# Kernel optimization log

Measured on AMD Instinct MI355X. Metric: run time of the kernel, lower is better.

Reference implementation:

```python
import jax, jax.numpy as jnp
import numpy as np

N, IN_DIM, OUT_DIM, H, EDGE_DIM, E = 4096, 256, 256, 4, 64, 131072
HEAD_DIM = OUT_DIM // H
LN_EPS = 1e-5


def setup_inputs() -> dict:
    key = jax.random.key(0)
    ks = jax.random.split(key, 12)
    s_in = 1.0 / np.sqrt(IN_DIM)
    s_e = 1.0 / np.sqrt(EDGE_DIM)
    s_o = 1.0 / np.sqrt(OUT_DIM)
    return {
        "node_features": jax.random.normal(ks[0], (N, IN_DIM), jnp.float32),
        "adj_matrix": jax.random.uniform(ks[1], (N, N), jnp.float32),
        "edge_features": jax.random.normal(ks[2], (E, EDGE_DIM), jnp.float32),
        "edge_indices": jax.random.randint(ks[3], (E, 2), 0, N, dtype=jnp.int32),
        "Wq": jax.random.normal(ks[4], (IN_DIM, OUT_DIM), jnp.float32) * s_in,
        "bq": jnp.zeros((OUT_DIM,), jnp.float32),
        "Wk": jax.random.normal(ks[5], (IN_DIM, OUT_DIM), jnp.float32) * s_in,
        "bk": jnp.zeros((OUT_DIM,), jnp.float32),
        "Wv": jax.random.normal(ks[6], (IN_DIM, OUT_DIM), jnp.float32) * s_in,
        "bv": jnp.zeros((OUT_DIM,), jnp.float32),
        "We": jax.random.normal(ks[7], (EDGE_DIM, H), jnp.float32) * s_e,
        "be": jnp.zeros((H,), jnp.float32),
        "Wo": jax.random.normal(ks[8], (OUT_DIM, OUT_DIM), jnp.float32) * s_o,
        "bo": jnp.zeros((OUT_DIM,), jnp.float32),
        "ln_gamma": jnp.ones((OUT_DIM,), jnp.float32),
        "ln_beta": jnp.zeros((OUT_DIM,), jnp.float32),
    }


def reference(node_features, adj_matrix, edge_features, edge_indices,
              Wq, bq, Wk, bk, Wv, bv, We, be, Wo, bo, ln_gamma, ln_beta):
    n = node_features.shape[0]
    scale = np.float32(1.0 / np.sqrt(HEAD_DIM))
    Q = (node_features @ Wq + bq).reshape(n, H, HEAD_DIM)
    K = (node_features @ Wk + bk).reshape(n, H, HEAD_DIM)
    V = (node_features @ Wv + bv).reshape(n, H, HEAD_DIM)
    # scores[n, m, h] = <Q[n,h], K[m,h]> / sqrt(d)
    scores = jnp.einsum('nhd,mhd->nmh', Q, K) * scale
    scores = scores + adj_matrix[:, :, None] * 10.0
    # per-edge additive attention bias, scatter-added into (src, tgt) slots
    edge_attn = edge_features[:, :EDGE_DIM] @ We + be  # [E, H]
    scores = scores.at[edge_indices[:, 0], edge_indices[:, 1]].add(edge_attn)
    attn = jax.nn.softmax(scores, axis=1)  # over key nodes m
    out = jnp.einsum('nmh,mhd->nhd', attn, V).reshape(n, OUT_DIM)
    out = out @ Wo + bo
    x = out + node_features  # residual
    mu = jnp.mean(x, axis=-1, keepdims=True)
    var = jnp.mean((x - mu) ** 2, axis=-1, keepdims=True)
    return ln_gamma * (x - mu) * jax.lax.rsqrt(var + LN_EPS) + ln_beta
```

## Files before the change

kernel.cpp:

```cpp
#include <hip/hip_runtime.h>
#include <hip/hip_bf16.h>

typedef unsigned short u16;
typedef unsigned int u32;
typedef __attribute__((ext_vector_type(8))) short bf8;
typedef __attribute__((ext_vector_type(4))) float f4;

#define SCALE 0.125f
#define LN_EPS 1e-5f
#define WS_NEED 18485504UL

__device__ __forceinline__ float bf2f(u16 u) {
    union { u32 i; float f; } x; x.i = ((u32)u) << 16; return x.f;
}
__device__ __forceinline__ u16 f2bf(float f) {
    union { u32 i; float f; } x; x.f = f;
    u32 i = x.i;
    return (u16)((i + 0x7FFFu + ((i >> 16) & 1u)) >> 16);
}
__device__ __forceinline__ float ldf(const void* p, long i, int isf) {
    return isf ? ((const float*)p)[i] : bf2f(((const u16*)p)[i]);
}

__global__ void k_zero(int* p, int n) {
    int i = blockIdx.x * 256 + threadIdx.x;
    if (i < n) p[i] = 0;
}

__global__ void k_detect(const u32* __restrict__ w, int nwords, int* flag) {
    int hits = 0;
    for (int i = blockIdx.x * 256 + threadIdx.x; i < nwords; i += 64 * 256) {
        u32 v = w[i];
        if (((v >> 7) & 0xFFu) == 0xFFu) hits++;
        if (((v >> 23) & 0xFFu) == 0xFFu) hits++;
    }
    if (hits) atomicOr(flag, 1);
}

__global__ __launch_bounds__(256) void k_cvt_small(
    const void* bq, const void* bk, const void* bv, const void* bo,
    const void* g, const void* bt, const void* We, const void* be,
    u16* __restrict__ SB, const int* __restrict__ flag)
{
    int isf = flag[0];
    int t = threadIdx.x;
    SB[0 * 256 + t] = isf ? f2bf(((const float*)bq)[t]) : ((const u16*)bq)[t];
    SB[1 * 256 + t] = isf ? f2bf(((const float*)bk)[t]) : ((const u16*)bk)[t];
    SB[2 * 256 + t] = isf ? f2bf(((const float*)bv)[t]) : ((const u16*)bv)[t];
    SB[3 * 256 + t] = isf ? f2bf(((const float*)bo)[t]) : ((const u16*)bo)[t];
    SB[4 * 256 + t] = isf ? f2bf(((const float*)g)[t])  : ((const u16*)g)[t];
    SB[5 * 256 + t] = isf ? f2bf(((const float*)bt)[t]) : ((const u16*)bt)[t];
    SB[6 * 256 + t] = isf ? f2bf(((const float*)We)[t]) : ((const u16*)We)[t];
    if (t < 4)
        SB[7 * 256 + t] = isf ? f2bf(((const float*)be)[t]) : ((const u16*)be)[t];
}

__global__ __launch_bounds__(256) void k_transpose(const void* __restrict__ Wq,
    const void* __restrict__ Wk, const void* __restrict__ Wv, const void* __restrict__ Wo,
    u16* __restrict__ out, const int* __restrict__ flag)
{
    __shared__ u16 tile[32][33];
    int isf = flag[0];
    const void* src = blockIdx.z == 0 ? Wq : blockIdx.z == 1 ? Wk : blockIdx.z == 2 ? Wv : Wo;
    u16* dst = out + blockIdx.z * 65536;
    int r0 = blockIdx.x * 32, c0 = blockIdx.y * 32;
    int lr = threadIdx.x >> 5, lc = threadIdx.x & 31;
    #pragma unroll
    for (int rr = 0; rr < 4; rr++) {
        int r = rr * 8 + lr;
        long idx = (long)(r0 + r) * 256 + c0 + lc;
        tile[r][lc] = isf ? f2bf(((const float*)src)[idx]) : ((const u16*)src)[idx];
    }
    __syncthreads();
    #pragma unroll
    for (int rr = 0; rr < 4; rr++) {
        int r = rr * 8 + lr;
        dst[(c0 + r) * 256 + r0 + lc] = tile[lc][r];
    }
}

__global__ __launch_bounds__(256) void k_qkv(const void* __restrict__ X,
    const u16* __restrict__ WT, const u16* __restrict__ SB,
    u16* __restrict__ Qo, u16* __restrict__ Kp, u16* __restrict__ Vp,
    const int* __restrict__ flag)
{
    int tid = threadIdx.x, wave = tid >> 6, lane = tid & 63, quad = lane >> 4, c = lane & 15;
    int m0 = blockIdx.x * 16;
    int isf = flag[0];

    bf8 af[8];
    if (isf) {
        const float* Xf = (const float*)X;
        #pragma unroll
        for (int ks = 0; ks < 8; ks++) {
            const float* p = Xf + (long)(m0 + c) * 256 + ks * 32 + quad * 8;
            f4 a = *(const f4*)p, b = *(const f4*)(p + 4);
            bf8 t;
            #pragma unroll
            for (int j = 0; j < 4; j++) { t[j] = (short)f2bf(a[j]); t[j + 4] = (short)f2bf(b[j]); }
            af[ks] = t;
        }
    } else {
        #pragma unroll
        for (int ks = 0; ks < 8; ks++)
            af[ks] = *(const bf8*)((const u16*)X + (long)(m0 + c) * 256 + ks * 32 + quad * 8);
    }

    for (int which = 0; which < 3; which++) {
        const u16* Wp = WT + which * 65536;
        const u16* bias = SB + which * 256;

        f4 acc[4];
        #pragma unroll
        for (int t = 0; t < 4; t++) acc[t] = (f4){0.f, 0.f, 0.f, 0.f};

        #pragma unroll
        for (int ks = 0; ks < 8; ks++) {
            #pragma unroll
            for (int t = 0; t < 4; t++) {
                bf8 bfr = *(const bf8*)(Wp + (wave * 64 + t * 16 + c) * 256 + ks * 32 + quad * 8);
                acc[t] = __builtin_amdgcn_mfma_f32_16x16x32_bf16(af[ks], bfr, acc[t], 0, 0, 0);
            }
        }
        #pragma unroll
        for (int t = 0; t < 4; t++) {
            int n = wave * 64 + t * 16 + c;
            float bb = bf2f(bias[n]);
            #pragma unroll
            for (int r = 0; r < 4; r++) {
                int row = m0 + quad * 4 + r;
                float v = acc[t][r] + bb;
                u16 bv16 = f2bf(v);
                if (which == 0) {
                    Qo[(long)row * 256 + n] = bv16;
                } else if (which == 1) {
                    int mt = row >> 6, tk = (row >> 4) & 3, ck = row & 15;
                    int hh = n >> 6, kw = (n >> 5) & 1, q = (n >> 3) & 3, j = n & 7;
                    long idx = ((long)(((mt * 4 + hh) * 4 + tk) * 2 + kw) * 64 + q * 16 + ck) * 8 + j;
                    Kp[idx] = bv16;
                } else {
                    int hh = n >> 6, t2 = (n >> 4) & 3, c2 = n & 15;
                    int mt = row >> 6, mo = row & 63, hf = mo >> 5, q = (mo >> 3) & 3, j = mo & 7;
                    long idx = ((long)(((mt * 4 + hh) * 4 + t2) * 2 + hf) * 64 + q * 16 + c2) * 8 + j;
                    Vp[idx] = bv16;
                }
            }
        }
    }
}

__global__ void k_count(const int* __restrict__ EI, int* bcnt) {
    int e = blockIdx.x * 256 + threadIdx.x;
    int src = EI[2 * e], tgt = EI[2 * e + 1];
    atomicAdd(&bcnt[(src >> 4) * 64 + (tgt >> 6)], 1);
}

__global__ __launch_bounds__(256) void k_scan(const int* __restrict__ cntin,
                                              int* __restrict__ bptr, int* __restrict__ nextc)
{
    __shared__ int tot[256], base_l[256];
    int tid = threadIdx.x;
    int s = 0;
    int loc[64];
    #pragma unroll
    for (int j = 0; j < 64; j++) { loc[j] = cntin[tid * 64 + j]; s += loc[j]; }
    tot[tid] = s;
    __syncthreads();
    if (tid == 0) {
        int run = 0;
        for (int i = 0; i < 256; i++) { int t = tot[i]; base_l[i] = run; run += t; }
        bptr[16384] = run;
    }
    __syncthreads();
    int b = base_l[tid];
    #pragma unroll
    for (int j = 0; j < 64; j++) { bptr[tid * 64 + j] = b; nextc[tid * 64 + j] = b; b += loc[j]; }
}

__global__ __launch_bounds__(256) void k_fill(const void* __restrict__ EF,
    const int* __restrict__ EI, const u16* __restrict__ SB,
    int* __restrict__ nextc, int* __restrict__ csr_tq, float* __restrict__ csr_b,
    const int* __restrict__ flag)
{
    __shared__ float Wl[64][4];
    __shared__ float bel[4];
    int tid = threadIdx.x;
    int isf = flag[0];
    Wl[tid >> 2][tid & 3] = bf2f(SB[6 * 256 + tid]);
    if (tid < 4) bel[tid] = bf2f(SB[7 * 256 + tid]);
    __syncthreads();
    int e = blockIdx.x * 256 + tid;
    int src = EI[2 * e], tgt = EI[2 * e + 1];
    float ea0 = bel[0], ea1 = bel[1], ea2 = bel[2], ea3 = bel[3];
    if (isf) {
        const float* Ff = (const float*)EF + (long)e * 64;
        for (int d0 = 0; d0 < 64; d0 += 4) {
            f4 v = *(const f4*)(Ff + d0);
            #pragma unroll
            for (int j = 0; j < 4; j++) {
                float f = v[j];
                ea0 += f * Wl[d0 + j][0];
                ea1 += f * Wl[d0 + j][1];
                ea2 += f * Wl[d0 + j][2];
                ea3 += f * Wl[d0 + j][3];
            }
        }
    } else {
        const u16* Fb = (const u16*)EF + (long)e * 64;
        for (int d0 = 0; d0 < 64; d0 += 8) {
            bf8 v8 = *(const bf8*)(Fb + d0);
            #pragma unroll
            for (int j = 0; j < 8; j++) {
                float f = bf2f((u16)v8[j]);
                ea0 += f * Wl[d0 + j][0];
                ea1 += f * Wl[d0 + j][1];
                ea2 += f * Wl[d0 + j][2];
                ea3 += f * Wl[d0 + j][3];
            }
        }
    }
    int bucket = (src >> 4) * 64 + (tgt >> 6);
    int pos = atomicAdd(&nextc[bucket], 1);
    csr_tq[pos] = ((src & 15) << 16) | tgt;
    f4 bb = {ea0, ea1, ea2, ea3};
    *(f4*)(csr_b + (long)pos * 4) = bb;
}

__global__ __launch_bounds__(64, 4) void k_flash(
    const u16* __restrict__ Qb, const u16* __restrict__ Kp, const u16* __restrict__ Vp,
    const void* __restrict__ adj, const int* __restrict__ bptr,
    const int* __restrict__ csr_tq, const float* __restrict__ csr_b,
    float* __restrict__ AOacc, float* __restrict__ Lacc, const int* __restrict__ flag)
{
    __shared__ alignas(16) float EBs[16][68];

    int lane = threadIdx.x, quad = lane >> 4, c = lane & 15;
    int qt = blockIdx.x, h = blockIdx.y, ks = blockIdx.z;
    int n0 = qt * 16;
    int isf = flag[0];

    bf8 qf[2];
    #pragma unroll
    for (int kw = 0; kw < 2; kw++)
        qf[kw] = *(const bf8*)(Qb + (long)(n0 + c) * 256 + h * 64 + kw * 32 + quad * 8);

    float l_run = 0.f;
    f4 Oacc[4];
    #pragma unroll
    for (int t = 0; t < 4; t++) Oacc[t] = (f4){0.f, 0.f, 0.f, 0.f};

    int zr = lane >> 2, zc0 = (lane & 3) * 16;
    int addrA = ((2 * (quad & 1)) * 16 + c) * 4;
    int addrB = addrA + 64;
    int selLo = quad < 2;

    int mt0 = ks * 16;

    f4 z = (f4){0.f, 0.f, 0.f, 0.f};
    #pragma unroll
    for (int k = 0; k < 4; k++) *(f4*)(&EBs[zr][zc0 + k * 4]) = z;

    f4 adjc[4];
    #pragma unroll
    for (int t = 0; t < 4; t++) {
        int col = mt0 * 64 + t * 16 + quad * 4;
        if (isf) {
            adjc[t] = *(const f4*)((const float*)adj + (long)(n0 + c) * 4096 + col);
        } else {
            ushort4 u = *(const ushort4*)((const u16*)adj + (long)(n0 + c) * 4096 + col);
            adjc[t] = (f4){bf2f(u.x), bf2f(u.y), bf2f(u.z), bf2f(u.w)};
        }
    }

    int bi0 = 0, bi1 = 0, tq = 0, has = 0;
    float ebv = 0.f;

    for (int rel = 0; rel < 16; rel++) {
        int mt = mt0 + rel;

        if ((rel & 3) == 0) {
            int b = qt * 64 + mt;
            bi0 = bptr[b]; bi1 = bptr[b + 4];
            int ie = bi0 + lane;
            has = ie < bi1;
            tq = 0; ebv = 0.f;
            if (has) { tq = csr_tq[ie]; ebv = csr_b[(long)ie * 4 + h]; }
        }

        if (has && (((tq & 0xFFFF) >> 6) == mt))
            atomicAdd(&EBs[tq >> 16][tq & 63], ebv);
        if (bi1 > bi0 + 64) {
            for (int i = bi0 + 64 + lane; i < bi1; i += 64) {
                int tq2 = csr_tq[i];
                if (((tq2 & 0xFFFF) >> 6) == mt)
                    atomicAdd(&EBs[tq2 >> 16][tq2 & 63], csr_b[(long)i * 4 + h]);
            }
        }

        float sv[4][4];
        #pragma unroll
        for (int t = 0; t < 4; t++) {
            f4 acc = (f4){0.f, 0.f, 0.f, 0.f};
            #pragma unroll
            for (int kw = 0; kw < 2; kw++) {
                bf8 kfr = *(const bf8*)(Kp + ((long)(((mt * 4 + h) * 4 + t) * 2 + kw) * 64 + lane) * 8);
                acc = __builtin_amdgcn_mfma_f32_16x16x32_bf16(kfr, qf[kw], acc, 0, 0, 0);
            }
            #pragma unroll
            for (int r = 0; r < 4; r++)
                sv[t][r] = acc[r] * SCALE + adjc[t][r] * 10.f;
        }

        if (rel < 15) {
            int m0n = (mt + 1) * 64;
            #pragma unroll
            for (int t = 0; t < 4; t++) {
                int col = m0n + t * 16 + quad * 4;
                if (isf) {
                    adjc[t] = *(const f4*)((const float*)adj + (long)(n0 + c) * 4096 + col);
                } else {
                    ushort4 u = *(const ushort4*)((const u16*)adj + (long)(n0 + c) * 4096 + col);
                    adjc[t] = (f4){bf2f(u.x), bf2f(u.y), bf2f(u.z), bf2f(u.w)};
                }
            }
        }

        #pragma unroll
        for (int t = 0; t < 4; t++) {
            f4 e = *(const f4*)(&EBs[c][t * 16 + quad * 4]);
            #pragma unroll
            for (int r = 0; r < 4; r++) sv[t][r] += e[r];
        }
        #pragma unroll
        for (int k = 0; k < 4; k++) *(f4*)(&EBs[zr][zc0 + k * 4]) = z;

        u32 pw[8];
        float s = 0.f;
        #pragma unroll
        for (int t = 0; t < 4; t++) {
            float p0 = __expf(sv[t][0]);
            float p1 = __expf(sv[t][1]);
            float p2 = __expf(sv[t][2]);
            float p3 = __expf(sv[t][3]);
            s += (p0 + p1) + (p2 + p3);
            pw[2 * t]     = (u32)f2bf(p0) | ((u32)f2bf(p1) << 16);
            pw[2 * t + 1] = (u32)f2bf(p2) | ((u32)f2bf(p3) << 16);
        }
        l_run += s;

        union PF { u32 w[4]; bf8 v; } pf0, pf1;
        {
            u32 a00 = (u32)__builtin_amdgcn_ds_bpermute(addrA, (int)pw[0]);
            u32 a10 = (u32)__builtin_amdgcn_ds_bpermute(addrA, (int)pw[2]);
            u32 a01 = (u32)__builtin_amdgcn_ds_bpermute(addrA, (int)pw[1]);
            u32 a11 = (u32)__builtin_amdgcn_ds_bpermute(addrA, (int)pw[3]);
            u32 b00 = (u32)__builtin_amdgcn_ds_bpermute(addrB, (int)pw[0]);
            u32 b10 = (u32)__builtin_amdgcn_ds_bpermute(addrB, (int)pw[2]);
            u32 b01 = (u32)__builtin_amdgcn_ds_bpermute(addrB, (int)pw[1]);
            u32 b11 = (u32)__builtin_amdgcn_ds_bpermute(addrB, (int)pw[3]);
            pf0.w[0] = selLo ? a00 : a10;
            pf0.w[1] = selLo ? a01 : a11;
            pf0.w[2] = selLo ? b00 : b10;
            pf0.w[3] = selLo ? b01 : b11;
            u32 c00 = (u32)__builtin_amdgcn_ds_bpermute(addrA, (int)pw[4]);
            u32 c10 = (u32)__builtin_amdgcn_ds_bpermute(addrA, (int)pw[6]);
            u32 c01 = (u32)__builtin_amdgcn_ds_bpermute(addrA, (int)pw[5]);
            u32 c11 = (u32)__builtin_amdgcn_ds_bpermute(addrA, (int)pw[7]);
            u32 d00 = (u32)__builtin_amdgcn_ds_bpermute(addrB, (int)pw[4]);
            u32 d10 = (u32)__builtin_amdgcn_ds_bpermute(addrB, (int)pw[6]);
            u32 d01 = (u32)__builtin_amdgcn_ds_bpermute(addrB, (int)pw[5]);
            u32 d11 = (u32)__builtin_amdgcn_ds_bpermute(addrB, (int)pw[7]);
            pf1.w[0] = selLo ? c00 : c10;
            pf1.w[1] = selLo ? c01 : c11;
            pf1.w[2] = selLo ? d00 : d10;
            pf1.w[3] = selLo ? d01 : d11;
        }

        #pragma unroll
        for (int t = 0; t < 4; t++) {
            f4 o = Oacc[t];
            bf8 v0 = *(const bf8*)(Vp + ((long)(((mt * 4 + h) * 4 + t) * 2 + 0) * 64 + lane) * 8);
            o = __builtin_amdgcn_mfma_f32_16x16x32_bf16(pf0.v, v0, o, 0, 0, 0);
            bf8 v1 = *(const bf8*)(Vp + ((long)(((mt * 4 + h) * 4 + t) * 2 + 1) * 64 + lane) * 8);
            o = __builtin_amdgcn_mfma_f32_16x16x32_bf16(pf1.v, v1, o, 0, 0, 0);
            Oacc[t] = o;
        }
    }

    l_run += __shfl_xor(l_run, 16);
    l_run += __shfl_xor(l_run, 32);

    #pragma unroll
    for (int t = 0; t < 4; t++) {
        #pragma unroll
        for (int r = 0; r < 4; r++) {
            int q = quad * 4 + r;
            atomicAdd(&AOacc[(long)(n0 + q) * 256 + h * 64 + t * 16 + c], Oacc[t][r]);
        }
    }
    if (quad == 0)
        atomicAdd(&Lacc[(n0 + c) * 4 + h], l_run);
}

__global__ __launch_bounds__(256) void k_reduce(const float* __restrict__ AOacc,
    const float* __restrict__ Lacc, u16* __restrict__ AOb)
{
    int n = blockIdx.x, hd = threadIdx.x;
    float L = Lacc[n * 4 + (hd >> 6)];
    AOb[(long)n * 256 + hd] = f2bf(AOacc[(long)n * 256 + hd] / L);
}

__global__ __launch_bounds__(256) void k_outln(
    const u16* __restrict__ AOb, const u16* __restrict__ WoT, const u16* __restrict__ SB,
    const void* __restrict__ Xin, const void* __restrict__ gv, const void* __restrict__ bv,
    void* __restrict__ out, const int* __restrict__ flag)
{
    __shared__ float Xl[16][257];
    __shared__ float ps[16][17], pss[16][17];
    __shared__ float mu_l[16], ri_l[16];
    int tid = threadIdx.x, wave = tid >> 6, lane = tid & 63, quad = lane >> 4, c = lane & 15;
    int m0 = blockIdx.x * 16;
    int isf = flag[0];

    bf8 af[8];
    #pragma unroll
    for (int ks = 0; ks < 8; ks++)
        af[ks] = *(const bf8*)(AOb + (long)(m0 + c) * 256 + ks * 32 + quad * 8);

    f4 acc[4];
    #pragma unroll
    for (int t = 0; t < 4; t++) acc[t] = (f4){0.f, 0.f, 0.f, 0.f};

    #pragma unroll
    for (int ks = 0; ks < 8; ks++) {
        #pragma unroll
        for (int t = 0; t < 4; t++) {
            bf8 bfr = *(const bf8*)(WoT + (wave * 64 + t * 16 + c) * 256 + ks * 32 + quad * 8);
            acc[t] = __builtin_amdgcn_mfma_f32_16x16x32_bf16(af[ks], bfr, acc[t], 0, 0, 0);
        }
    }
    #pragma unroll
    for (int t = 0; t < 4; t++) {
        int n = wave * 64 + t * 16 + c;
        float bb = bf2f(SB[3 * 256 + n]);
        #pragma unroll
        for (int r = 0; r < 4; r++) {
            int q = quad * 4 + r;
            float res = ldf(Xin, (long)(m0 + q) * 256 + n, isf);
            Xl[q][n] = acc[t][r] + bb + res;
        }
    }
    __syncthreads();
    int q = tid >> 4, i = tid & 15;
    float s = 0.f, ss = 0.f;
    #pragma unroll
    for (int j = 0; j < 16; j++) { float v = Xl[q][i * 16 + j]; s += v; ss += v * v; }
    ps[q][i] = s; pss[q][i] = ss;
    __syncthreads();
    if (tid < 16) {
        float s2 = 0.f, ss2 = 0.f;
        #pragma unroll
        for (int i2 = 0; i2 < 16; i2++) { s2 += ps[tid][i2]; ss2 += pss[tid][i2]; }
        float mu = s2 * (1.f / 256.f);
        float var = ss2 * (1.f / 256.f) - mu * mu;
        mu_l[tid] = mu;
        ri_l[tid] = rsqrtf(var + LN_EPS);
    }
    __syncthreads();
    float mu = mu_l[q], ri = ri_l[q];
    #pragma unroll
    for (int j = 0; j < 16; j++) {
        int n2 = i * 16 + j;
        float v = (Xl[q][n2] - mu) * ri;
        float g = ldf(gv, n2, isf), bt = ldf(bv, n2, isf);
        float y = g * v + bt;
        long oidx = (long)(m0 + q) * 256 + n2;
        if (isf) ((float*)out)[oidx] = y;
        else     ((u16*)out)[oidx] = f2bf(y);
    }
}

extern "C" void kernel_launch(void* const* d_in, const int* in_sizes, int n_in,
                              void* d_out, int out_size, void* d_ws, size_t ws_size,
                              hipStream_t stream)
{
    const void* node = d_in[0];
    const void* adj  = d_in[1];
    const void* ef   = d_in[2];
    const int*  ei   = (const int*)d_in[3];
    const void* Wq = d_in[4];  const void* bq = d_in[5];
    const void* Wk = d_in[6];  const void* bk = d_in[7];
    const void* Wv = d_in[8];  const void* bv = d_in[9];
    const void* We = d_in[10]; const void* be = d_in[11];
    const void* Wo = d_in[12]; const void* bo = d_in[13];
    const void* gamma = d_in[14];
    const void* beta  = d_in[15];

    if (ws_size < WS_NEED) return;

    char* ws = (char*)d_ws;
    u16*   WT     = (u16*)(ws + 0);
    u16*   Qb     = (u16*)(ws + 524288);
    u16*   AOb    = (u16*)(ws + 524288);
    u16*   Kp     = (u16*)(ws + 2621440);
    u16*   Vp     = (u16*)(ws + 4718592);
    float* AOacc  = (float*)(ws + 6815744);
    float* Lacc   = (float*)(ws + 11010048);
    u16*   SB     = (u16*)(ws + 15728640);
    int*   bcnt   = (int*)(ws + 15732736);
    int*   flag   = bcnt + 16384;
    int*   bptr   = (int*)(ws + 15798400);
    int*   csr_tq = (int*)(ws + 15864064);
    float* csr_b  = (float*)(ws + 16388352);

    k_zero<<<65, 256, 0, stream>>>(bcnt, 16416);
    k_zero<<<4160, 256, 0, stream>>>((int*)AOacc, 1064960);
    k_detect<<<64, 256, 0, stream>>>((const u32*)node, 524288, flag);
    k_cvt_small<<<1, 256, 0, stream>>>(bq, bk, bv, bo, gamma, beta, We, be, SB, flag);
    k_transpose<<<dim3(8, 8, 4), 256, 0, stream>>>(Wq, Wk, Wv, Wo, WT, flag);
    k_qkv<<<256, 256, 0, stream>>>(node, WT, SB, Qb, Kp, Vp, flag);
    k_count<<<512, 256, 0, stream>>>(ei, bcnt);
    k_scan<<<1, 256, 0, stream>>>(bcnt, bptr, bcnt);
    k_fill<<<512, 256, 0, stream>>>(ef, ei, SB, bcnt, csr_tq, csr_b, flag);
    k_flash<<<dim3(256, 4, 4), 64, 0, stream>>>(Qb, Kp, Vp, adj, bptr, csr_tq, csr_b,
                                                AOacc, Lacc, flag);
    k_reduce<<<4096, 256, 0, stream>>>(AOacc, Lacc, AOb);
    k_outln<<<256, 256, 0, stream>>>(AOb, WT + 3 * 65536, SB, node, gamma, beta, d_out, flag);
}
```

Baseline: 293.7 us.

## Fuse setup kernels, merge QKV with edge fill, prefetch K tiles in flash

Merges several small launches: the two zeroing kernels, format detection with edge counting, bias conversion into the transpose, and the QKV projection with the CSR edge fill. The softmax normalisation divide is folded into the output-projection kernel, so the separate reduce pass and its bf16 intermediate go away. The flash kernel now loads the next key tile's fragments into registers one iteration ahead instead of loading right before the MFMAs. The aim is to cut launch overhead and serialization and to hide K load latency, at the cost of more registers in the flash kernel and heterogeneous blocks in the fused kernels.

New measurement: 301.0 us. 2.5% more time.

```diff
diff --git a/kernel.cpp b/kernel.cpp
--- a/kernel.cpp
+++ b/kernel.cpp
@@ -22,45 +22,53 @@
     return isf ? ((const float*)p)[i] : bf2f(((const u16*)p)[i]);
 }
 
-__global__ void k_zero(int* p, int n) {
+__global__ void k_zero2(int* __restrict__ a, int na, int* __restrict__ b, int nb) {
     int i = blockIdx.x * 256 + threadIdx.x;
-    if (i < n) p[i] = 0;
-}
-
-__global__ void k_detect(const u32* __restrict__ w, int nwords, int* flag) {
-    int hits = 0;
-    for (int i = blockIdx.x * 256 + threadIdx.x; i < nwords; i += 64 * 256) {
-        u32 v = w[i];
-        if (((v >> 7) & 0xFFu) == 0xFFu) hits++;
-        if (((v >> 23) & 0xFFu) == 0xFFu) hits++;
-    }
-    if (hits) atomicOr(flag, 1);
-}
-
-__global__ __launch_bounds__(256) void k_cvt_small(
-    const void* bq, const void* bk, const void* bv, const void* bo,
-    const void* g, const void* bt, const void* We, const void* be,
-    u16* __restrict__ SB, const int* __restrict__ flag)
-{
-    int isf = flag[0];
-    int t = threadIdx.x;
-    SB[0 * 256 + t] = isf ? f2bf(((const float*)bq)[t]) : ((const u16*)bq)[t];
-    SB[1 * 256 + t] = isf ? f2bf(((const float*)bk)[t]) : ((const u16*)bk)[t];
-    SB[2 * 256 + t] = isf ? f2bf(((const float*)bv)[t]) : ((const u16*)bv)[t];
-    SB[3 * 256 + t] = isf ? f2bf(((const float*)bo)[t]) : ((const u16*)bo)[t];
-    SB[4 * 256 + t] = isf ? f2bf(((const float*)g)[t])  : ((const u16*)g)[t];
-    SB[5 * 256 + t] = isf ? f2bf(((const float*)bt)[t]) : ((const u16*)bt)[t];
-    SB[6 * 256 + t] = isf ? f2bf(((const float*)We)[t]) : ((const u16*)We)[t];
-    if (t < 4)
-        SB[7 * 256 + t] = isf ? f2bf(((const float*)be)[t]) : ((const u16*)be)[t];
+    if (i < na) a[i] = 0;
+    else if (i - na < nb) b[i - na] = 0;
+}
+
+__global__ void k_detcnt(const u32* __restrict__ w, int nwords, int* __restrict__ flag,
+                         const int* __restrict__ EI, int* __restrict__ bcnt) {
+    int bx = blockIdx.x;
+    if (bx < 64) {
+        int hits = 0;
+        for (int i = bx * 256 + threadIdx.x; i < nwords; i += 64 * 256) {
+            u32 v = w[i];
+            if (((v >> 7) & 0xFFu) == 0xFFu) hits++;
+            if (((v >> 23) & 0xFFu) == 0xFFu) hits++;
+        }
+        if (hits) atomicOr(flag, 1);
+    } else {
+        int e = (bx - 64) * 256 + threadIdx.x;
+        int src = EI[2 * e], tgt = EI[2 * e + 1];
+        atomicAdd(&bcnt[(src >> 4) * 64 + (tgt >> 6)], 1);
+    }
 }
 
 __global__ __launch_bounds__(256) void k_transpose(const void* __restrict__ Wq,
     const void* __restrict__ Wk, const void* __restrict__ Wv, const void* __restrict__ Wo,
-    u16* __restrict__ out, const int* __restrict__ flag)
+    u16* __restrict__ out, const int* __restrict__ flag,
+    const void* bq, const void* bk, const void* bv, const void* bo,
+    const void* g, const void* bt, const void* We, const void* be, u16* __restrict__ SB)
 {
     __shared__ u16 tile[32][33];
     int isf = flag[0];
+    if (blockIdx.z == 4) {
+        if (blockIdx.x == 0 && blockIdx.y == 0) {
+            int t = threadIdx.x;
+            SB[0 * 256 + t] = isf ? f2bf(((const float*)bq)[t]) : ((const u16*)bq)[t];
+            SB[1 * 256 + t] = isf ? f2bf(((const float*)bk)[t]) : ((const u16*)bk)[t];
+            SB[2 * 256 + t] = isf ? f2bf(((const float*)bv)[t]) : ((const u16*)bv)[t];
+            SB[3 * 256 + t] = isf ? f2bf(((const float*)bo)[t]) : ((const u16*)bo)[t];
+            SB[4 * 256 + t] = isf ? f2bf(((const float*)g)[t])  : ((const u16*)g)[t];
+            SB[5 * 256 + t] = isf ? f2bf(((const float*)bt)[t]) : ((const u16*)bt)[t];
+            SB[6 * 256 + t] = isf ? f2bf(((const float*)We)[t]) : ((const u16*)We)[t];
+            if (t < 4)
+                SB[7 * 256 + t] = isf ? f2bf(((const float*)be)[t]) : ((const u16*)be)[t];
+        }
+        return;
+    }
     const void* src = blockIdx.z == 0 ? Wq : blockIdx.z == 1 ? Wk : blockIdx.z == 2 ? Wv : Wo;
     u16* dst = out + blockIdx.z * 65536;
     int r0 = blockIdx.x * 32, c0 = blockIdx.y * 32;
@@ -77,82 +85,6 @@
         int r = rr * 8 + lr;
         dst[(c0 + r) * 256 + r0 + lc] = tile[lc][r];
     }
-}
-
-__global__ __launch_bounds__(256) void k_qkv(const void* __restrict__ X,
-    const u16* __restrict__ WT, const u16* __restrict__ SB,
-    u16* __restrict__ Qo, u16* __restrict__ Kp, u16* __restrict__ Vp,
-    const int* __restrict__ flag)
-{
-    int tid = threadIdx.x, wave = tid >> 6, lane = tid & 63, quad = lane >> 4, c = lane & 15;
-    int m0 = blockIdx.x * 16;
-    int isf = flag[0];
-
-    bf8 af[8];
-    if (isf) {
-        const float* Xf = (const float*)X;
-        #pragma unroll
-        for (int ks = 0; ks < 8; ks++) {
-            const float* p = Xf + (long)(m0 + c) * 256 + ks * 32 + quad * 8;
-            f4 a = *(const f4*)p, b = *(const f4*)(p + 4);
-            bf8 t;
-            #pragma unroll
-            for (int j = 0; j < 4; j++) { t[j] = (short)f2bf(a[j]); t[j + 4] = (short)f2bf(b[j]); }
-            af[ks] = t;
-        }
-    } else {
-        #pragma unroll
-        for (int ks = 0; ks < 8; ks++)
-            af[ks] = *(const bf8*)((const u16*)X + (long)(m0 + c) * 256 + ks * 32 + quad * 8);
-    }
-
-    for (int which = 0; which < 3; which++) {
-        const u16* Wp = WT + which * 65536;
-        const u16* bias = SB + which * 256;
-
-        f4 acc[4];
-        #pragma unroll
-        for (int t = 0; t < 4; t++) acc[t] = (f4){0.f, 0.f, 0.f, 0.f};
-
-        #pragma unroll
-        for (int ks = 0; ks < 8; ks++) {
-            #pragma unroll
-            for (int t = 0; t < 4; t++) {
-                bf8 bfr = *(const bf8*)(Wp + (wave * 64 + t * 16 + c) * 256 + ks * 32 + quad * 8);
-                acc[t] = __builtin_amdgcn_mfma_f32_16x16x32_bf16(af[ks], bfr, acc[t], 0, 0, 0);
-            }
-        }
-        #pragma unroll
-        for (int t = 0; t < 4; t++) {
-            int n = wave * 64 + t * 16 + c;
-            float bb = bf2f(bias[n]);
-            #pragma unroll
-            for (int r = 0; r < 4; r++) {
-                int row = m0 + quad * 4 + r;
-                float v = acc[t][r] + bb;
-                u16 bv16 = f2bf(v);
-                if (which == 0) {
-                    Qo[(long)row * 256 + n] = bv16;
-                } else if (which == 1) {
-                    int mt = row >> 6, tk = (row >> 4) & 3, ck = row & 15;
-                    int hh = n >> 6, kw = (n >> 5) & 1, q = (n >> 3) & 3, j = n & 7;
-                    long idx = ((long)(((mt * 4 + hh) * 4 + tk) * 2 + kw) * 64 + q * 16 + ck) * 8 + j;
-                    Kp[idx] = bv16;
-                } else {
-                    int hh = n >> 6, t2 = (n >> 4) & 3, c2 = n & 15;
-                    int mt = row >> 6, mo = row & 63, hf = mo >> 5, q = (mo >> 3) & 3, j = mo & 7;
-                    long idx = ((long)(((mt * 4 + hh) * 4 + t2) * 2 + hf) * 64 + q * 16 + c2) * 8 + j;
-                    Vp[idx] = bv16;
-                }
-            }
-        }
-    }
-}
-
-__global__ void k_count(const int* __restrict__ EI, int* bcnt) {
-    int e = blockIdx.x * 256 + threadIdx.x;
-    int src = EI[2 * e], tgt = EI[2 * e + 1];
-    atomicAdd(&bcnt[(src >> 4) * 64 + (tgt >> 6)], 1);
 }
 
 __global__ __launch_bounds__(256) void k_scan(const int* __restrict__ cntin,
@@ -177,8 +109,10 @@
     for (int j = 0; j < 64; j++) { bptr[tid * 64 + j] = b; nextc[tid * 64 + j] = b; b += loc[j]; }
 }
 
-__global__ __launch_bounds__(256) void k_fill(const void* __restrict__ EF,
-    const int* __restrict__ EI, const u16* __restrict__ SB,
+__global__ __launch_bounds__(256) void k_qkvfill(const void* __restrict__ X,
+    const u16* __restrict__ WT, const u16* __restrict__ SB,
+    u16* __restrict__ Qo, u16* __restrict__ Kp, u16* __restrict__ Vp,
+    const void* __restrict__ EF, const int* __restrict__ EI,
     int* __restrict__ nextc, int* __restrict__ csr_tq, float* __restrict__ csr_b,
     const int* __restrict__ flag)
 {
@@ -186,44 +120,110 @@
     __shared__ float bel[4];
     int tid = threadIdx.x;
     int isf = flag[0];
-    Wl[tid >> 2][tid & 3] = bf2f(SB[6 * 256 + tid]);
-    if (tid < 4) bel[tid] = bf2f(SB[7 * 256 + tid]);
-    __syncthreads();
-    int e = blockIdx.x * 256 + tid;
-    int src = EI[2 * e], tgt = EI[2 * e + 1];
-    float ea0 = bel[0], ea1 = bel[1], ea2 = bel[2], ea3 = bel[3];
-    if (isf) {
-        const float* Ff = (const float*)EF + (long)e * 64;
-        for (int d0 = 0; d0 < 64; d0 += 4) {
-            f4 v = *(const f4*)(Ff + d0);
-            #pragma unroll
-            for (int j = 0; j < 4; j++) {
-                float f = v[j];
-                ea0 += f * Wl[d0 + j][0];
-                ea1 += f * Wl[d0 + j][1];
-                ea2 += f * Wl[d0 + j][2];
-                ea3 += f * Wl[d0 + j][3];
+
+    if (blockIdx.x < 256) {
+        int wave = tid >> 6, lane = tid & 63, quad = lane >> 4, c = lane & 15;
+        int m0 = blockIdx.x * 16;
+
+        bf8 af[8];
+        if (isf) {
+            const float* Xf = (const float*)X;
+            #pragma unroll
+            for (int ks = 0; ks < 8; ks++) {
+                const float* p = Xf + (long)(m0 + c) * 256 + ks * 32 + quad * 8;
+                f4 a = *(const f4*)p, b = *(const f4*)(p + 4);
+                bf8 t;
+                #pragma unroll
+                for (int j = 0; j < 4; j++) { t[j] = (short)f2bf(a[j]); t[j + 4] = (short)f2bf(b[j]); }
+                af[ks] = t;
+            }
+        } else {
+            #pragma unroll
+            for (int ks = 0; ks < 8; ks++)
+                af[ks] = *(const bf8*)((const u16*)X + (long)(m0 + c) * 256 + ks * 32 + quad * 8);
+        }
+
+        for (int which = 0; which < 3; which++) {
+            const u16* Wp = WT + which * 65536;
+            const u16* bias = SB + which * 256;
+
+            f4 acc[4];
+            #pragma unroll
+            for (int t = 0; t < 4; t++) acc[t] = (f4){0.f, 0.f, 0.f, 0.f};
+
+            #pragma unroll
+            for (int ks = 0; ks < 8; ks++) {
+                #pragma unroll
+                for (int t = 0; t < 4; t++) {
+                    bf8 bfr = *(const bf8*)(Wp + (wave * 64 + t * 16 + c) * 256 + ks * 32 + quad * 8);
+                    acc[t] = __builtin_amdgcn_mfma_f32_16x16x32_bf16(af[ks], bfr, acc[t], 0, 0, 0);
+                }
+            }
+            #pragma unroll
+            for (int t = 0; t < 4; t++) {
+                int n = wave * 64 + t * 16 + c;
+                float bb = bf2f(bias[n]);
+                #pragma unroll
+                for (int r = 0; r < 4; r++) {
+                    int row = m0 + quad * 4 + r;
+                    float v = acc[t][r] + bb;
+                    u16 bv16 = f2bf(v);
+                    if (which == 0) {
+                        Qo[(long)row * 256 + n] = bv16;
+                    } else if (which == 1) {
+                        int mt = row >> 6, tk = (row >> 4) & 3, ck = row & 15;
+                        int hh = n >> 6, kw = (n >> 5) & 1, q = (n >> 3) & 3, j = n & 7;
+                        long idx = ((long)(((mt * 4 + hh) * 4 + tk) * 2 + kw) * 64 + q * 16 + ck) * 8 + j;
+                        Kp[idx] = bv16;
+                    } else {
+                        int hh = n >> 6, t2 = (n >> 4) & 3, c2 = n & 15;
+                        int mt = row >> 6, mo = row & 63, hf = mo >> 5, q = (mo >> 3) & 3, j = mo & 7;
+                        long idx = ((long)(((mt * 4 + hh) * 4 + t2) * 2 + hf) * 64 + q * 16 + c2) * 8 + j;
+                        Vp[idx] = bv16;
+                    }
+                }
             }
         }
     } else {
-        const u16* Fb = (const u16*)EF + (long)e * 64;
-        for (int d0 = 0; d0 < 64; d0 += 8) {
-            bf8 v8 = *(const bf8*)(Fb + d0);
-            #pragma unroll
-            for (int j = 0; j < 8; j++) {
-                float f = bf2f((u16)v8[j]);
-                ea0 += f * Wl[d0 + j][0];
-                ea1 += f * Wl[d0 + j][1];
-                ea2 += f * Wl[d0 + j][2];
-                ea3 += f * Wl[d0 + j][3];
-            }
-        }
-    }
-    int bucket = (src >> 4) * 64 + (tgt >> 6);
-    int pos = atomicAdd(&nextc[bucket], 1);
-    csr_tq[pos] = ((src & 15) << 16) | tgt;
-    f4 bb = {ea0, ea1, ea2, ea3};
-    *(f4*)(csr_b + (long)pos * 4) = bb;
+        Wl[tid >> 2][tid & 3] = bf2f(SB[6 * 256 + tid]);
+        if (tid < 4) bel[tid] = bf2f(SB[7 * 256 + tid]);
+        __syncthreads();
+        int e = (blockIdx.x - 256) * 256 + tid;
+        int src = EI[2 * e], tgt = EI[2 * e + 1];
+        float ea0 = bel[0], ea1 = bel[1], ea2 = bel[2], ea3 = bel[3];
+        if (isf) {
+            const float* Ff = (const float*)EF + (long)e * 64;
+            for (int d0 = 0; d0 < 64; d0 += 4) {
+                f4 v = *(const f4*)(Ff + d0);
+                #pragma unroll
+                for (int j = 0; j < 4; j++) {
+                    float f = v[j];
+                    ea0 += f * Wl[d0 + j][0];
+                    ea1 += f * Wl[d0 + j][1];
+                    ea2 += f * Wl[d0 + j][2];
+                    ea3 += f * Wl[d0 + j][3];
+                }
+            }
+        } else {
+            const u16* Fb = (const u16*)EF + (long)e * 64;
+            for (int d0 = 0; d0 < 64; d0 += 8) {
+                bf8 v8 = *(const bf8*)(Fb + d0);
+                #pragma unroll
+                for (int j = 0; j < 8; j++) {
+                    float f = bf2f((u16)v8[j]);
+                    ea0 += f * Wl[d0 + j][0];
+                    ea1 += f * Wl[d0 + j][1];
+                    ea2 += f * Wl[d0 + j][2];
+                    ea3 += f * Wl[d0 + j][3];
+                }
+            }
+        }
+        int bucket = (src >> 4) * 64 + (tgt >> 6);
+        int pos = atomicAdd(&nextc[bucket], 1);
+        csr_tq[pos] = ((src & 15) << 16) | tgt;
+        f4 bb = {ea0, ea1, ea2, ea3};
+        *(f4*)(csr_b + (long)pos * 4) = bb;
+    }
 }
 
 __global__ __launch_bounds__(64, 4) void k_flash(
@@ -271,6 +271,12 @@
             adjc[t] = (f4){bf2f(u.x), bf2f(u.y), bf2f(u.z), bf2f(u.w)};
         }
     }
+    bf8 kf[4][2];
+    #pragma unroll
+    for (int t = 0; t < 4; t++)
+        #pragma unroll
+        for (int kw = 0; kw < 2; kw++)
+            kf[t][kw] = *(const bf8*)(Kp + ((long)(((mt0 * 4 + h) * 4 + t) * 2 + kw) * 64 + lane) * 8);
 
     int bi0 = 0, bi1 = 0, tq = 0, has = 0;
     float ebv = 0.f;
@@ -301,18 +307,21 @@
         #pragma unroll
         for (int t = 0; t < 4; t++) {
             f4 acc = (f4){0.f, 0.f, 0.f, 0.f};
-            #pragma unroll
-            for (int kw = 0; kw < 2; kw++) {
-                bf8 kfr = *(const bf8*)(Kp + ((long)(((mt * 4 + h) * 4 + t) * 2 + kw) * 64 + lane) * 8);
-                acc = __builtin_amdgcn_mfma_f32_16x16x32_bf16(kfr, qf[kw], acc, 0, 0, 0);
-            }
+            acc = __builtin_amdgcn_mfma_f32_16x16x32_bf16(kf[t][0], qf[0], acc, 0, 0, 0);
+            acc = __builtin_amdgcn_mfma_f32_16x16x32_bf16(kf[t][1], qf[1], acc, 0, 0, 0);
             #pragma unroll
             for (int r = 0; r < 4; r++)
                 sv[t][r] = acc[r] * SCALE + adjc[t][r] * 10.f;
         }
 
         if (rel < 15) {
-            int m0n = (mt + 1) * 64;
+            int mtn = mt + 1;
+            #pragma unroll
+            for (int t = 0; t < 4; t++)
+                #pragma unroll
+                for (int kw = 0; kw < 2; kw++)
+                    kf[t][kw] = *(const bf8*)(Kp + ((long)(((mtn * 4 + h) * 4 + t) * 2 + kw) * 64 + lane) * 8);
+            int m0n = mtn * 64;
             #pragma unroll
             for (int t = 0; t < 4; t++) {
                 int col = m0n + t * 16 + quad * 4;
@@ -402,16 +411,9 @@
         atomicAdd(&Lacc[(n0 + c) * 4 + h], l_run);
 }
 
-__global__ __launch_bounds__(256) void k_reduce(const float* __restrict__ AOacc,
-    const float* __restrict__ Lacc, u16* __restrict__ AOb)
-{
-    int n = blockIdx.x, hd = threadIdx.x;
-    float L = Lacc[n * 4 + (hd >> 6)];
-    AOb[(long)n * 256 + hd] = f2bf(AOacc[(long)n * 256 + hd] / L);
-}
-
 __global__ __launch_bounds__(256) void k_outln(
-    const u16* __restrict__ AOb, const u16* __restrict__ WoT, const u16* __restrict__ SB,
+    const float* __restrict__ AOacc, const float* __restrict__ Lacc,
+    const u16* __restrict__ WoT, const u16* __restrict__ SB,
     const void* __restrict__ Xin, const void* __restrict__ gv, const void* __restrict__ bv,
     void* __restrict__ out, const int* __restrict__ flag)
 {
@@ -422,10 +424,22 @@
     int m0 = blockIdx.x * 16;
     int isf = flag[0];
 
+    int rowa = m0 + c;
+    float l4[4];
+    #pragma unroll
+    for (int hh = 0; hh < 4; hh++) l4[hh] = Lacc[rowa * 4 + hh];
+
     bf8 af[8];
     #pragma unroll
-    for (int ks = 0; ks < 8; ks++)
-        af[ks] = *(const bf8*)(AOb + (long)(m0 + c) * 256 + ks * 32 + quad * 8);
+    for (int ks = 0; ks < 8; ks++) {
+        const float* pa = AOacc + (long)rowa * 256 + ks * 32 + quad * 8;
+        f4 a = *(const f4*)pa, b = *(const f4*)(pa + 4);
+        float L = l4[ks >> 1];
+        bf8 t;
+        #pragma unroll
+        for (int j = 0; j < 4; j++) { t[j] = (short)f2bf(a[j] / L); t[j + 4] = (short)f2bf(b[j] / L); }
+        af[ks] = t;
+    }
 
     f4 acc[4];
     #pragma unroll
@@ -501,7 +515,6 @@
     char* ws = (char*)d_ws;
     u16*   WT     = (u16*)(ws + 0);
     u16*   Qb     = (u16*)(ws + 524288);
-    u16*   AOb    = (u16*)(ws + 524288);
     u16*   Kp     = (u16*)(ws + 2621440);
     u16*   Vp     = (u16*)(ws + 4718592);
     float* AOacc  = (float*)(ws + 6815744);
@@ -513,17 +526,15 @@
     int*   csr_tq = (int*)(ws + 15864064);
     float* csr_b  = (float*)(ws + 16388352);
 
-    k_zero<<<65, 256, 0, stream>>>(bcnt, 16416);
-    k_zero<<<4160, 256, 0, stream>>>((int*)AOacc, 1064960);
-    k_detect<<<64, 256, 0, stream>>>((const u32*)node, 524288, flag);
-    k_cvt_small<<<1, 256, 0, stream>>>(bq, bk, bv, bo, gamma, beta, We, be, SB, flag);
-    k_transpose<<<dim3(8, 8, 4), 256, 0, stream>>>(Wq, Wk, Wv, Wo, WT, flag);
-    k_qkv<<<256, 256, 0, stream>>>(node, WT, SB, Qb, Kp, Vp, flag);
-    k_count<<<512, 256, 0, stream>>>(ei, bcnt);
+    k_zero2<<<4225, 256, 0, stream>>>(bcnt, 16416, (int*)AOacc, 1064960);
+    k_detcnt<<<576, 256, 0, stream>>>((const u32*)node, 524288, flag, ei, bcnt);
+    k_transpose<<<dim3(8, 8, 5), 256, 0, stream>>>(Wq, Wk, Wv, Wo, WT, flag,
+                                                   bq, bk, bv, bo, gamma, beta, We, be, SB);
     k_scan<<<1, 256, 0, stream>>>(bcnt, bptr, bcnt);
-    k_fill<<<512, 256, 0, stream>>>(ef, ei, SB, bcnt, csr_tq, csr_b, flag);
+    k_qkvfill<<<768, 256, 0, stream>>>(node, WT, SB, Qb, Kp, Vp,
+                                       ef, ei, bcnt, csr_tq, csr_b, flag);
     k_flash<<<dim3(256, 4, 4), 64, 0, stream>>>(Qb, Kp, Vp, adj, bptr, csr_tq, csr_b,
                                                 AOacc, Lacc, flag);
-    k_reduce<<<4096, 256, 0, stream>>>(AOacc, Lacc, AOb);
-    k_outln<<<256, 256, 0, stream>>>(AOb, WT + 3 * 65536, SB, node, gamma, beta, d_out, flag);
-}
+    k_outln<<<256, 256, 0, stream>>>(AOacc, Lacc, WT + 3 * 65536, SB, node, gamma, beta,
+                                     d_out, flag);
+}
```
